# Kernel optimization log

Measured on AMD Instinct MI355X. Metric: run time of the kernel, lower is better.

## Reference

```python
import jax, jax.numpy as jnp
import numpy as np

N_HEADS = 16
EPS = 1e-5  # torch nn.LayerNorm default


def layernorm(x, g, b):
    mu = x.mean(-1, keepdims=True)
    var = ((x - mu) ** 2).mean(-1, keepdims=True)
    return (x - mu) * jax.lax.rsqrt(var + EPS) * g + b


def setup_inputs() -> dict:
    V, D, Dff, L, S, B = 32000, 1024, 4096, 6, 2048, 1
    key = jax.random.key(0)
    ks = jax.random.split(key, 12)
    std = 0.02  # GPT-2 init
    nrm = lambda k, shp: jax.random.normal(k, shp, jnp.float32) * std
    return {
        "tokens": jax.random.randint(ks[0], (B, S), 0, V),
        "tok_emb": nrm(ks[1], (V, D)),          # tied with lm head
        "pos_emb": nrm(ks[2], (S, D)),
        "Wq": nrm(ks[3], (L, D, D)), "bq": jnp.zeros((L, D)),
        "Wk": nrm(ks[4], (L, D, D)), "bk": jnp.zeros((L, D)),
        "Wv": nrm(ks[5], (L, D, D)), "bv": jnp.zeros((L, D)),
        "Wo": nrm(ks[6], (L, D, D)), "bo": jnp.zeros((L, D)),
        "ln1_g": jnp.ones((L, D)), "ln1_b": jnp.zeros((L, D)),
        "ln2_g": jnp.ones((L, D)), "ln2_b": jnp.zeros((L, D)),
        "W1": nrm(ks[7], (L, D, Dff)), "b1": jnp.zeros((L, Dff)),
        "W2": nrm(ks[8], (L, Dff, D)), "b2": jnp.zeros((L, D)),
        "lnf_g": jnp.ones((D,)), "lnf_b": jnp.zeros((D,)),
    }


def reference(tokens, tok_emb, pos_emb, Wq, bq, Wk, bk, Wv, bv, Wo, bo,
              ln1_g, ln1_b, ln2_g, ln2_b, W1, b1, W2, b2, lnf_g, lnf_b):
    B, S = tokens.shape
    D = tok_emb.shape[1]
    dk = D // N_HEADS
    scale = 1.0 / np.sqrt(dk)

    x = tok_emb[tokens] + pos_emb[:S][None]           # (B,S,D); dropout p=0 -> identity
    causal = jnp.tril(jnp.ones((S, S), bool))

    def block(x, p):
        wq, bq_, wk, bk_, wv, bv_, wo, bo_, g1, b1_, g2, b2_, w1, bf1, w2, bf2 = p
        # --- attention sublayer (pre-norm) ---
        h = layernorm(x, g1, b1_)
        q = (h @ wq + bq_).reshape(B, S, N_HEADS, dk)
        k = (h @ wk + bk_).reshape(B, S, N_HEADS, dk)
        v = (h @ wv + bv_).reshape(B, S, N_HEADS, dk)
        scores = jnp.einsum('bqhd,bkhd->bhqk', q, k) * scale
        scores = jnp.where(causal, scores, -jnp.inf)   # masked_fill(mask==0, -inf)
        attn = jax.nn.softmax(scores, axis=-1)
        ctx = jnp.einsum('bhqk,bkhd->bqhd', attn, v).reshape(B, S, D)
        x = x + ctx @ wo + bo_
        # --- FFN sublayer (pre-norm) ---
        h = layernorm(x, g2, b2_)
        x = x + jax.nn.gelu(h @ w1 + bf1, approximate=False) @ w2 + bf2
        return x, None

    x, _ = jax.lax.scan(
        block, x,
        (Wq, bq, Wk, bk, Wv, bv, Wo, bo, ln1_g, ln1_b, ln2_g, ln2_b, W1, b1, W2, b2))
    x = layernorm(x, lnf_g, lnf_b)
    logits = x @ tok_emb.T                             # tied lm head (no bias)
    return logits
```

## Files before the change

kernel.cpp:

```cpp
#include <hip/hip_runtime.h>
#include <hip/hip_bf16.h>
#include <cstdint>
#include <cstddef>


typedef __attribute__((ext_vector_type(4))) float  f32x4;
typedef __attribute__((ext_vector_type(8))) __bf16 bf16x8;
typedef __attribute__((ext_vector_type(4))) __bf16 bf16x4;

#define S_LEN 2048
#define DMODEL 1024
#define DFF 4096
#define NLAYER 6
#define NHEAD 16
#define DK 64
#define VOCAB 32000
#define MN (S_LEN * DMODEL)

__device__ __forceinline__ void gload_lds16(const void* g, void* l) {
    __builtin_amdgcn_global_load_lds(
        (__attribute__((address_space(1))) void*)(void*)(g),
        (__attribute__((address_space(3))) void*)(l), 16, 0, 0);
}

__device__ __forceinline__ void tr64_body(
    const float* __restrict__ inp, __bf16* __restrict__ outp,
    int K, int N, int n0, int k0, int t) {
    __shared__ float tile[64][65];
    const int lc = t & 15, rr = t >> 4;
#pragma unroll
    for (int i = 0; i < 4; ++i) {
        float4 v = *(const float4*)&inp[(size_t)(k0 + rr + i * 16) * N + n0 + lc * 4];
        tile[rr + i * 16][lc * 4 + 0] = v.x;
        tile[rr + i * 16][lc * 4 + 1] = v.y;
        tile[rr + i * 16][lc * 4 + 2] = v.z;
        tile[rr + i * 16][lc * 4 + 3] = v.w;
    }
    __syncthreads();
    const int a = t & 7, b = t >> 3;
#pragma unroll
    for (int j = 0; j < 2; ++j) {
        const int n = b + j * 32;
        bf16x8 o;
#pragma unroll
        for (int e = 0; e < 8; ++e) o[e] = (__bf16)tile[a * 8 + e][n];
        *(bf16x8*)&outp[(size_t)(n0 + n) * K + k0 + a * 8] = o;
    }
}

__global__ __launch_bounds__(256) void transpose_cvt64(
    const float* __restrict__ in, __bf16* __restrict__ out,
    int K, int N, size_t in_lstride, size_t out_lstride) {
    tr64_body(in + blockIdx.z * in_lstride, out + blockIdx.z * out_lstride,
              K, N, blockIdx.x * 64, blockIdx.y * 64, threadIdx.x);
}

__global__ __launch_bounds__(256) void transpose_qkvo(
    const float* __restrict__ Wq, const float* __restrict__ Wk,
    const float* __restrict__ Wv, const float* __restrict__ Wo,
    __bf16* __restrict__ wqkv_t, __bf16* __restrict__ wo_t) {
    const int z = blockIdx.z, mat = z & 3, l = z >> 2;
    const float* src =
        (mat == 0 ? Wq : mat == 1 ? Wk : mat == 2 ? Wv : Wo) +
        (size_t)l * 1024 * 1024;
    __bf16* dst = (mat < 3)
        ? wqkv_t + (size_t)l * 3072 * 1024 + (size_t)mat * 1024 * 1024
        : wo_t + (size_t)l * 1024 * 1024;
    tr64_body(src, dst, 1024, 1024, blockIdx.x * 64, blockIdx.y * 64, threadIdx.x);
}

__global__ __launch_bounds__(256) void cvt_bf16(
    const float* __restrict__ in, __bf16* __restrict__ out, long n4) {
    long i = (long)blockIdx.x * 256 + threadIdx.x;
    if (i >= n4) return;
    float4 v = ((const float4*)in)[i];
    bf16x4 o = {(__bf16)v.x, (__bf16)v.y, (__bf16)v.z, (__bf16)v.w};
    ((bf16x4*)out)[i] = o;
}

template <int NPART, int EMBED>
__global__ __launch_bounds__(256) void ln_kernel(
    float* __restrict__ x, const float* __restrict__ p,
    const float* __restrict__ g, const float* __restrict__ b,
    __bf16* __restrict__ out,
    const int* __restrict__ tokens, const float* __restrict__ te,
    const float* __restrict__ pe) {
    const int row = blockIdx.x, t = threadIdx.x;
    float4 v;
    if (EMBED) {
        const int tok = tokens[row];
        float4 a = ((const float4*)(te + (size_t)tok * DMODEL))[t];
        float4 q = ((const float4*)(pe + (size_t)row * DMODEL))[t];
        v = float4{a.x + q.x, a.y + q.y, a.z + q.z, a.w + q.w};
        ((float4*)(x + (size_t)row * DMODEL))[t] = v;
    } else {
        v = ((const float4*)(x + (size_t)row * DMODEL))[t];
    }
    if (NPART == 2) {
        float4 a0 = ((const float4*)(p + (size_t)row * DMODEL))[t];
        float4 a1 = ((const float4*)(p + MN + (size_t)row * DMODEL))[t];
        v.x += a0.x + a1.x;
        v.y += a0.y + a1.y;
        v.z += a0.z + a1.z;
        v.w += a0.w + a1.w;
        ((float4*)(x + (size_t)row * DMODEL))[t] = v;
    }
    float s  = v.x + v.y + v.z + v.w;
    float s2 = v.x * v.x + v.y * v.y + v.z * v.z + v.w * v.w;
#pragma unroll
    for (int off = 1; off < 64; off <<= 1) {
        s  += __shfl_xor(s, off);
        s2 += __shfl_xor(s2, off);
    }
    __shared__ float ss[4], ss2[4];
    const int wave = t >> 6;
    if ((t & 63) == 0) { ss[wave] = s; ss2[wave] = s2; }
    __syncthreads();
    s  = ss[0] + ss[1] + ss[2] + ss[3];
    s2 = ss2[0] + ss2[1] + ss2[2] + ss2[3];
    const float mu  = s * (1.0f / DMODEL);
    const float var = s2 * (1.0f / DMODEL) - mu * mu;
    const float rstd = rsqrtf(var + 1e-5f);
    float4 gg = ((const float4*)g)[t];
    float4 bb = ((const float4*)b)[t];
    __bf16* o = out + (size_t)row * DMODEL + t * 4;
    o[0] = (__bf16)((v.x - mu) * rstd * gg.x + bb.x);
    o[1] = (__bf16)((v.y - mu) * rstd * gg.y + bb.y);
    o[2] = (__bf16)((v.z - mu) * rstd * gg.z + bb.z);
    o[3] = (__bf16)((v.w - mu) * rstd * gg.w + bb.w);
}

template <int BM, int BN, int BK, int SPLITK, int MODE, int XCD>
__global__ __launch_bounds__(256) void gemm_tiled(
    const __bf16* __restrict__ A, const __bf16* __restrict__ BT,
    int M, int N, int K,
    const float* __restrict__ bias,
    float* __restrict__ fout,
    __bf16* __restrict__ bfout,
    __bf16* __restrict__ qb, __bf16* __restrict__ kb, __bf16* __restrict__ vb,
    const float* __restrict__ bq, const float* __restrict__ bk,
    const float* __restrict__ bv) {
    constexpr int SLOTS = BK / 8;
    constexpr int SH    = (BK == 64) ? 0 : 1;
    constexpr int RPC   = 2048 / BK;
    constexpr int ACH_A = BM / RPC;
    constexpr int ACH_B = BN / RPC;
    constexpr int LOADS = ACH_A + ACH_B;
    constexpr int MR = BM / 32;
    constexpr int NR = BN / 32;
    constexpr int KS = BK / 32;
    __shared__ alignas(16) __bf16 As[2][BM * BK];
    __shared__ alignas(16) __bf16 Bs[2][BN * BK];
    const int t = threadIdx.x;
    const int wave = t >> 6, lane = t & 63;
    const int wr = wave >> 1, wc = wave & 1;
    const int lg = lane >> 4, lr = lane & 15;

    int bx = blockIdx.x, by = blockIdx.y;
    if (XCD) {
        const int nwg = gridDim.x * gridDim.y;
        const int wgid = by * gridDim.x + bx;
        const int sw = (wgid & 7) * (nwg >> 3) + (wgid >> 3);
        bx = sw % gridDim.x;
        by = sw / gridDim.x;
    }
    const int row0 = bx * BM, col0 = by * BN;
    const int kz = (SPLITK > 1) ? blockIdx.z : 0;
    const int Ksl = K / SPLITK;

    f32x4 acc[MR][NR];
#pragma unroll
    for (int i = 0; i < MR; i++)
#pragma unroll
        for (int j = 0; j < NR; j++) acc[i][j] = f32x4{0.f, 0.f, 0.f, 0.f};

    const int srow = t / SLOTS;
    const int sks = ((t % SLOTS) ^ ((srow >> SH) & (SLOTS - 1))) * 8;
    const __bf16* Ab = A + (size_t)(row0 + srow) * K + kz * Ksl + sks;
    const __bf16* Bb = BT + (size_t)(col0 + srow) * K + kz * Ksl + sks;

    const int nt = Ksl / BK;
#pragma unroll
    for (int ch = 0; ch < ACH_A; ++ch)
        gload_lds16(Ab + (size_t)ch * RPC * K, &As[0][ch * 2048 + wave * 512]);
#pragma unroll
    for (int ch = 0; ch < ACH_B; ++ch)
        gload_lds16(Bb + (size_t)ch * RPC * K, &Bs[0][ch * 2048 + wave * 512]);

    int c = 0;
    for (int T = 0; T < nt; ++T) {
        if (T + 1 < nt) {
            const int k0 = (T + 1) * BK;
#pragma unroll
            for (int ch = 0; ch < ACH_A; ++ch)
                gload_lds16(Ab + (size_t)ch * RPC * K + k0,
                            &As[c ^ 1][ch * 2048 + wave * 512]);
#pragma unroll
            for (int ch = 0; ch < ACH_B; ++ch)
                gload_lds16(Bb + (size_t)ch * RPC * K + k0,
                            &Bs[c ^ 1][ch * 2048 + wave * 512]);
            if constexpr (LOADS == 3)
                asm volatile("s_waitcnt vmcnt(3)" ::: "memory");
            else if constexpr (LOADS == 4)
                asm volatile("s_waitcnt vmcnt(4)" ::: "memory");
            else if constexpr (LOADS == 6)
                asm volatile("s_waitcnt vmcnt(6)" ::: "memory");
            else
                asm volatile("s_waitcnt vmcnt(8)" ::: "memory");
        } else {
            asm volatile("s_waitcnt vmcnt(0)" ::: "memory");
        }
        __builtin_amdgcn_s_barrier();
        asm volatile("" ::: "memory");

        bf16x8 af[MR][KS], bfr[NR][KS];
#pragma unroll
        for (int i = 0; i < MR; i++)
#pragma unroll
            for (int ks = 0; ks < KS; ks++) {
                const int row = wr * (BM / 2) + i * 16 + lr;
                const int ph = ((ks * 4 + lg) ^ ((row >> SH) & (SLOTS - 1)));
                af[i][ks] = *(const bf16x8*)&As[c][row * BK + ph * 8];
            }
#pragma unroll
        for (int j = 0; j < NR; j++)
#pragma unroll
            for (int ks = 0; ks < KS; ks++) {
                const int n = wc * (BN / 2) + j * 16 + lr;
                const int ph = ((ks * 4 + lg) ^ ((n >> SH) & (SLOTS - 1)));
                bfr[j][ks] = *(const bf16x8*)&Bs[c][n * BK + ph * 8];
            }
        __builtin_amdgcn_s_setprio(1);
#pragma unroll
        for (int i = 0; i < MR; i++)
#pragma unroll
            for (int j = 0; j < NR; j++)
#pragma unroll
                for (int ks = 0; ks < KS; ks++)
                    acc[i][j] = __builtin_amdgcn_mfma_f32_16x16x32_bf16(
                        af[i][ks], bfr[j][ks], acc[i][j], 0, 0, 0);
        __builtin_amdgcn_s_setprio(0);
        asm volatile("" ::: "memory");
        __builtin_amdgcn_s_barrier();
        c ^= 1;
    }

#pragma unroll
    for (int i = 0; i < MR; i++) {
#pragma unroll
        for (int j = 0; j < NR; j++) {
#pragma unroll
            for (int r = 0; r < 4; r++) {
                const int row = row0 + wr * (BM / 2) + i * 16 + lg * 4 + r;
                const int col = col0 + wc * (BN / 2) + j * 16 + lr;
                float v = acc[i][j][r];
                if (MODE == 0) {
                    const int sec = col >> 10, cn = col & 1023;
                    const int head = cn >> 6, d = cn & 63;
                    if (sec == 0) {
                        v = (v + bq[cn]) * 0.18033688011112042f;
                        qb[((size_t)head * S_LEN + row) * DK + d] = (__bf16)v;
                    } else if (sec == 1) {
                        v = v + bk[cn];
                        kb[((size_t)head * S_LEN + row) * DK + d] = (__bf16)v;
                    } else {
                        v = v + bv[cn];
                        vb[((size_t)head * DK + d) * S_LEN + row] = (__bf16)v;
                    }
                } else if (MODE == 2) {
                    const float gg = v + bias[col];
                    const float cgl = 0.5f * gg * (1.0f + erff(gg * 0.70710678118654752f));
                    bfout[(size_t)row * N + col] = (__bf16)cgl;
                } else if (MODE == 6) {
                    const float vv = v + (kz == 0 ? bias[col] : 0.f);
                    __builtin_nontemporal_store(
                        vv, &fout[(size_t)kz * MN + (size_t)row * N + col]);
                } else {
                    __builtin_nontemporal_store(v, &fout[(size_t)row * N + col]);
                }
            }
        }
    }
}

__global__ __launch_bounds__(256) void attn_kernel(
    const __bf16* __restrict__ q, const __bf16* __restrict__ k,
    const __bf16* __restrict__ vt, __bf16* __restrict__ ctx) {
    const int xb = blockIdx.x, head = blockIdx.y;
    const int t = threadIdx.x;
    const int wave = t >> 6, lane = t & 63;
    const int lg = lane >> 4, lr = lane & 15;
    const int rg = (wave < 2) ? (2 * xb + wave) : (127 - 2 * xb - (3 - wave));
    const int rowbase = rg * 16;
    const int tend = rg >> 3;

    const __bf16* qh = q + (size_t)head * S_LEN * DK;
    const __bf16* kh = k + (size_t)head * S_LEN * DK;
    const __bf16* vh = vt + (size_t)head * DK * S_LEN;

    __shared__ alignas(16) __bf16 pls[4][16 * 136];
    __bf16* pw = pls[wave];

    bf16x8 qf0 = *(const bf16x8*)&qh[(size_t)(rowbase + lr) * DK + lg * 8];
    bf16x8 qf1 = *(const bf16x8*)&qh[(size_t)(rowbase + lr) * DK + 32 + lg * 8];

    f32x4 oacc[4];
#pragma unroll
    for (int j = 0; j < 4; j++) oacc[j] = f32x4{0.f, 0.f, 0.f, 0.f};
    float m[4], l[4];
#pragma unroll
    for (int r = 0; r < 4; r++) { m[r] = -__builtin_inff(); l[r] = 0.f; }

    for (int tt = 0; tt <= tend; ++tt) {
        const int kv0 = tt * 128;
        f32x4 sc[8];
        __builtin_amdgcn_s_setprio(1);
#pragma unroll
        for (int jn = 0; jn < 8; jn++) {
            bf16x8 kf0 = *(const bf16x8*)&kh[(size_t)(kv0 + jn * 16 + lr) * DK + lg * 8];
            bf16x8 kf1 = *(const bf16x8*)&kh[(size_t)(kv0 + jn * 16 + lr) * DK + 32 + lg * 8];
            sc[jn] = __builtin_amdgcn_mfma_f32_16x16x32_bf16(
                qf0, kf0, f32x4{0.f, 0.f, 0.f, 0.f}, 0, 0, 0);
            sc[jn] = __builtin_amdgcn_mfma_f32_16x16x32_bf16(qf1, kf1, sc[jn], 0, 0, 0);
        }
        __builtin_amdgcn_s_setprio(0);

        if (tt == tend) {
#pragma unroll
            for (int jn = 0; jn < 8; jn++)
#pragma unroll
                for (int r = 0; r < 4; r++) {
                    const int qrow = rowbase + lg * 4 + r;
                    if (kv0 + jn * 16 + lr > qrow) sc[jn][r] = -__builtin_inff();
                }
        }

        float mt[4];
#pragma unroll
        for (int r = 0; r < 4; r++) {
            float a0 = fmaxf(fmaxf(sc[0][r], sc[1][r]), fmaxf(sc[2][r], sc[3][r]));
            float a1 = fmaxf(fmaxf(sc[4][r], sc[5][r]), fmaxf(sc[6][r], sc[7][r]));
            mt[r] = fmaxf(a0, a1);
        }
#pragma unroll
        for (int off = 1; off < 16; off <<= 1)
#pragma unroll
            for (int r = 0; r < 4; r++) mt[r] = fmaxf(mt[r], __shfl_xor(mt[r], off));

        float alpha[4], psum[4];
#pragma unroll
        for (int r = 0; r < 4; r++) {
            const float mn = fmaxf(m[r], mt[r]);
            alpha[r] = exp2f(m[r] - mn);
            m[r] = mn;
#pragma unroll
            for (int jn = 0; jn < 8; jn++) sc[jn][r] = exp2f(sc[jn][r] - mn);
            psum[r] = ((sc[0][r] + sc[1][r]) + (sc[2][r] + sc[3][r])) +
                      ((sc[4][r] + sc[5][r]) + (sc[6][r] + sc[7][r]));
        }
#pragma unroll
        for (int off = 1; off < 16; off <<= 1)
#pragma unroll
            for (int r = 0; r < 4; r++) psum[r] += __shfl_xor(psum[r], off);
#pragma unroll
        for (int r = 0; r < 4; r++) l[r] = l[r] * alpha[r] + psum[r];
#pragma unroll
        for (int j = 0; j < 4; j++)
#pragma unroll
            for (int r = 0; r < 4; r++) oacc[j][r] *= alpha[r];

#pragma unroll
        for (int r = 0; r < 4; r++)
#pragma unroll
            for (int jn = 0; jn < 8; jn++)
                pw[(lg * 4 + r) * 136 + jn * 16 + lr] = (__bf16)sc[jn][r];

        bf16x8 pf[4];
#pragma unroll
        for (int h = 0; h < 4; h++)
            pf[h] = *(const bf16x8*)&pw[lr * 136 + h * 32 + lg * 8];
        __builtin_amdgcn_s_setprio(1);
#pragma unroll
        for (int j = 0; j < 4; j++) {
#pragma unroll
            for (int h = 0; h < 4; h++) {
                bf16x8 vf = *(const bf16x8*)
                    &vh[(size_t)(j * 16 + lr) * S_LEN + kv0 + h * 32 + lg * 8];
                oacc[j] = __builtin_amdgcn_mfma_f32_16x16x32_bf16(
                    pf[h], vf, oacc[j], 0, 0, 0);
            }
        }
        __builtin_amdgcn_s_setprio(0);
    }

#pragma unroll
    for (int j = 0; j < 4; j++)
#pragma unroll
        for (int r = 0; r < 4; r++) {
            const int row = rowbase + lg * 4 + r;
            ctx[(size_t)row * DMODEL + head * DK + j * 16 + lr] =
                (__bf16)(oacc[j][r] / l[r]);
        }
}

extern "C" void kernel_launch(void* const* d_in, const int* in_sizes, int n_in,
                              void* d_out, int out_size, void* d_ws, size_t ws_size,
                              hipStream_t stream) {
    const int*   tokens  = (const int*)d_in[0];
    const float* tok_emb = (const float*)d_in[1];
    const float* pos_emb = (const float*)d_in[2];
    const float* Wq = (const float*)d_in[3];
    const float* bq = (const float*)d_in[4];
    const float* Wk = (const float*)d_in[5];
    const float* bk = (const float*)d_in[6];
    const float* Wv = (const float*)d_in[7];
    const float* bv = (const float*)d_in[8];
    const float* Wo = (const float*)d_in[9];
    const float* bo = (const float*)d_in[10];
    const float* ln1_g = (const float*)d_in[11];
    const float* ln1_b = (const float*)d_in[12];
    const float* ln2_g = (const float*)d_in[13];
    const float* ln2_b = (const float*)d_in[14];
    const float* W1 = (const float*)d_in[15];
    const float* b1 = (const float*)d_in[16];
    const float* W2 = (const float*)d_in[17];
    const float* b2 = (const float*)d_in[18];
    const float* lnf_g = (const float*)d_in[19];
    const float* lnf_b = (const float*)d_in[20];

    char* ws = (char*)d_ws;
    size_t off = 0;
    auto alloc = [&](size_t bytes) {
        char* p = ws + off;
        off = (off + bytes + 255) & ~(size_t)255;
        return p;
    };
    __bf16* wqkv_t = (__bf16*)alloc((size_t)NLAYER * 3072 * 1024 * 2);
    __bf16* wo_t   = (__bf16*)alloc((size_t)NLAYER * 1024 * 1024 * 2);
    __bf16* w1_t   = (__bf16*)alloc((size_t)NLAYER * 4096 * 1024 * 2);
    __bf16* w2_t   = (__bf16*)alloc((size_t)NLAYER * 1024 * 4096 * 2);
    __bf16* temb   = (__bf16*)alloc((size_t)VOCAB * DMODEL * 2);
    float*  x      = (float*)alloc((size_t)MN * 4);
    __bf16* h      = (__bf16*)alloc((size_t)MN * 2);
    __bf16* qbuf   = (__bf16*)alloc((size_t)MN * 2);
    __bf16* kbuf   = (__bf16*)alloc((size_t)MN * 2);
    __bf16* vbuf   = (__bf16*)alloc((size_t)MN * 2);
    __bf16* ctx    = (__bf16*)alloc((size_t)MN * 2);
    __bf16* ffn    = (__bf16*)alloc((size_t)S_LEN * DFF * 2);
    if (off > ws_size) return;

    float* pproj  = (float*)ffn;
    float* pffn2  = (float*)qbuf;

    const dim3 blk256(256);

    transpose_qkvo<<<dim3(16, 16, 4 * NLAYER), blk256, 0, stream>>>(
        Wq, Wk, Wv, Wo, wqkv_t, wo_t);
    transpose_cvt64<<<dim3(64, 16, NLAYER), blk256, 0, stream>>>(
        W1, w1_t, 1024, 4096, (size_t)1024 * 4096, (size_t)4096 * 1024);
    transpose_cvt64<<<dim3(16, 64, NLAYER), blk256, 0, stream>>>(
        W2, w2_t, 4096, 1024, (size_t)4096 * 1024, (size_t)1024 * 4096);
    cvt_bf16<<<dim3((VOCAB * DMODEL / 4 + 255) / 256), blk256, 0, stream>>>(
        tok_emb, temb, (long)VOCAB * DMODEL / 4);

    ln_kernel<0, 1><<<dim3(S_LEN), blk256, 0, stream>>>(
        x, nullptr, ln1_g, ln1_b, h, tokens, tok_emb, pos_emb);

    for (int l = 0; l < NLAYER; ++l) {
        gemm_tiled<128, 128, 64, 1, 0, 0><<<dim3(16, 24), blk256, 0, stream>>>(
            h, wqkv_t + (size_t)l * 3072 * 1024, S_LEN, 3072, 1024,
            nullptr, nullptr, nullptr, qbuf, kbuf, vbuf,
            bq + l * 1024, bk + l * 1024, bv + l * 1024);
        attn_kernel<<<dim3(32, NHEAD), blk256, 0, stream>>>(
            qbuf, kbuf, vbuf, ctx);
        gemm_tiled<64, 128, 64, 2, 6, 0><<<dim3(32, 8, 2), blk256, 0, stream>>>(
            ctx, wo_t + (size_t)l * 1024 * 1024, S_LEN, 1024, 1024,
            bo + l * 1024, pproj, nullptr, nullptr, nullptr, nullptr,
            nullptr, nullptr, nullptr);
        ln_kernel<2, 0><<<dim3(S_LEN), blk256, 0, stream>>>(
            x, pproj, ln2_g + l * 1024, ln2_b + l * 1024, h,
            nullptr, nullptr, nullptr);
        gemm_tiled<128, 128, 64, 1, 2, 0><<<dim3(16, 32), blk256, 0, stream>>>(
            h, w1_t + (size_t)l * 4096 * 1024, S_LEN, 4096, 1024,
            b1 + l * 4096, nullptr, ffn, nullptr, nullptr, nullptr,
            nullptr, nullptr, nullptr);
        gemm_tiled<64, 128, 64, 2, 6, 0><<<dim3(32, 8, 2), blk256, 0, stream>>>(
            ffn, w2_t + (size_t)l * 1024 * 4096, S_LEN, 1024, 4096,
            b2 + l * 1024, pffn2, nullptr, nullptr, nullptr, nullptr,
            nullptr, nullptr, nullptr);
        if (l + 1 < NLAYER) {
            ln_kernel<2, 0><<<dim3(S_LEN), blk256, 0, stream>>>(
                x, pffn2, ln1_g + (l + 1) * 1024, ln1_b + (l + 1) * 1024, h,
                nullptr, nullptr, nullptr);
        }
    }

    ln_kernel<2, 0><<<dim3(S_LEN), blk256, 0, stream>>>(
        x, pffn2, lnf_g, lnf_b, h, nullptr, nullptr, nullptr);
    gemm_tiled<128, 256, 32, 1, 3, 1><<<dim3(16, 125), blk256, 0, stream>>>(
        h, temb, S_LEN, VOCAB, 1024,
        nullptr, (float*)d_out, nullptr, nullptr, nullptr, nullptr,
        nullptr, nullptr, nullptr);
}
```

Measured before the change: 1.598 ms.

## Use one barrier per K-step in GEMM and XCD-swizzle attention blocks

The GEMM main loop is restructured. It loads the first tile up front, issues the prefetch of the next tile before computing the current one, and waits for all loads plus a single barrier after the compute. This drops the second per-iteration barrier and the LOADS-dependent partial vmcnt waits. Separately, the attention kernel remaps its block index so consecutive blocks spread across XCDs, which should improve cache locality per head. The full vmcnt(0) wait at the end of each step may expose some memory latency if the compute is shorter than the loads.

```diff
diff --git a/kernel.cpp b/kernel.cpp
--- a/kernel.cpp
+++ b/kernel.cpp
@@ -145,7 +145,6 @@
     constexpr int RPC   = 2048 / BK;
     constexpr int ACH_A = BM / RPC;
     constexpr int ACH_B = BN / RPC;
-    constexpr int LOADS = ACH_A + ACH_B;
     constexpr int MR = BM / 32;
     constexpr int NR = BN / 32;
     constexpr int KS = BK / 32;
@@ -180,38 +179,29 @@
     const __bf16* Bb = BT + (size_t)(col0 + srow) * K + kz * Ksl + sks;
 
     const int nt = Ksl / BK;
-#pragma unroll
-    for (int ch = 0; ch < ACH_A; ++ch)
-        gload_lds16(Ab + (size_t)ch * RPC * K, &As[0][ch * 2048 + wave * 512]);
-#pragma unroll
-    for (int ch = 0; ch < ACH_B; ++ch)
-        gload_lds16(Bb + (size_t)ch * RPC * K, &Bs[0][ch * 2048 + wave * 512]);
+    auto stage = [&](int T, int buf) {
+        const int k0 = T * BK;
+#pragma unroll
+        for (int ch = 0; ch < ACH_A; ++ch)
+            gload_lds16(Ab + (size_t)ch * RPC * K + k0,
+                        &As[buf][ch * 2048 + wave * 512]);
+#pragma unroll
+        for (int ch = 0; ch < ACH_B; ++ch)
+            gload_lds16(Bb + (size_t)ch * RPC * K + k0,
+                        &Bs[buf][ch * 2048 + wave * 512]);
+    };
+
+    stage(0, 0);
+    asm volatile("s_waitcnt vmcnt(0)" ::: "memory");
+    __builtin_amdgcn_s_barrier();
+    asm volatile("" ::: "memory");
 
     int c = 0;
     for (int T = 0; T < nt; ++T) {
         if (T + 1 < nt) {
-            const int k0 = (T + 1) * BK;
-#pragma unroll
-            for (int ch = 0; ch < ACH_A; ++ch)
-                gload_lds16(Ab + (size_t)ch * RPC * K + k0,
-                            &As[c ^ 1][ch * 2048 + wave * 512]);
-#pragma unroll
-            for (int ch = 0; ch < ACH_B; ++ch)
-                gload_lds16(Bb + (size_t)ch * RPC * K + k0,
-                            &Bs[c ^ 1][ch * 2048 + wave * 512]);
-            if constexpr (LOADS == 3)
-                asm volatile("s_waitcnt vmcnt(3)" ::: "memory");
-            else if constexpr (LOADS == 4)
-                asm volatile("s_waitcnt vmcnt(4)" ::: "memory");
-            else if constexpr (LOADS == 6)
-                asm volatile("s_waitcnt vmcnt(6)" ::: "memory");
-            else
-                asm volatile("s_waitcnt vmcnt(8)" ::: "memory");
-        } else {
-            asm volatile("s_waitcnt vmcnt(0)" ::: "memory");
-        }
-        __builtin_amdgcn_s_barrier();
-        asm volatile("" ::: "memory");
+            stage(T + 1, c ^ 1);
+            asm volatile("" ::: "memory");
+        }
 
         bf16x8 af[MR][KS], bfr[NR][KS];
 #pragma unroll
@@ -240,8 +230,12 @@
                     acc[i][j] = __builtin_amdgcn_mfma_f32_16x16x32_bf16(
                         af[i][ks], bfr[j][ks], acc[i][j], 0, 0, 0);
         __builtin_amdgcn_s_setprio(0);
-        asm volatile("" ::: "memory");
-        __builtin_amdgcn_s_barrier();
+
+        if (T + 1 < nt) {
+            asm volatile("s_waitcnt vmcnt(0)" ::: "memory");
+            __builtin_amdgcn_s_barrier();
+            asm volatile("" ::: "memory");
+        }
         c ^= 1;
     }
 
@@ -286,7 +280,9 @@
 __global__ __launch_bounds__(256) void attn_kernel(
     const __bf16* __restrict__ q, const __bf16* __restrict__ k,
     const __bf16* __restrict__ vt, __bf16* __restrict__ ctx) {
-    const int xb = blockIdx.x, head = blockIdx.y;
+    const int lin = blockIdx.y * 32 + blockIdx.x;
+    const int u = (lin & 7) * 64 + (lin >> 3);
+    const int head = u >> 5, xb = u & 31;
     const int t = threadIdx.x;
     const int wave = t >> 6, lane = t & 63;
     const int lg = lane >> 4, lr = lane & 15;
```

New measurement: 1.615 ms. About the same (+1.1%).

## Add dedicated 256x256 triple-buffered logits GEMM and remap attention block order

Applied to the files above, without the earlier changes.

Replaces the generic tiled GEMM for the tied LM-head logits with a specialized 512-thread kernel. It uses 256x256 tiles, triple-buffered LDS filled by direct global-to-LDS loads, swizzled LDS layout, and block-ID remapping so that blocks sharing A/B tiles are grouped per XCD. Attention blocks are also remapped so heads are spread across XCDs for better L2 locality. The larger tile raises per-CU reuse but leaves 1000 blocks at one block per CU, which risks tail imbalance and register pressure.

```diff
diff --git a/kernel.cpp b/kernel.cpp
--- a/kernel.cpp
+++ b/kernel.cpp
@@ -283,10 +283,102 @@
     }
 }
 
+__global__ __launch_bounds__(512, 1) void gemm_logits_p3(
+    const __bf16* __restrict__ A, const __bf16* __restrict__ BT,
+    float* __restrict__ fout) {
+    constexpr int K = 1024, N = VOCAB, NT = 32;
+    __shared__ alignas(16) __bf16 As[3][256 * 32];
+    __shared__ alignas(16) __bf16 Bs[3][256 * 32];
+    const int t = threadIdx.x;
+    const int wv = t >> 6, lane = t & 63;
+    const int wm = wv >> 2, wn = wv & 3;
+    const int lg = lane >> 4, lr = lane & 15;
+
+    const int wgid = blockIdx.x;
+    const int sw = (wgid & 7) * 125 + (wgid >> 3);
+    const int row0 = (sw & 7) * 256;
+    const int col0 = (sw >> 3) * 256;
+
+    const int srl = wv * 32 + (lane >> 2);
+    const int sks = ((lane & 3) ^ ((srl >> 1) & 3)) * 8;
+    const __bf16* Asrc = A + (size_t)(row0 + srl) * K + sks;
+    const __bf16* Bsrc = BT + (size_t)(col0 + srl) * K + sks;
+
+    auto stage = [&](int T, int buf) {
+        const int k0 = T * 32;
+        gload_lds16(Asrc + k0,              &As[buf][(wv * 32) * 32]);
+        gload_lds16(Asrc + (size_t)16 * K + k0, &As[buf][(wv * 32 + 16) * 32]);
+        gload_lds16(Bsrc + k0,              &Bs[buf][(wv * 32) * 32]);
+        gload_lds16(Bsrc + (size_t)16 * K + k0, &Bs[buf][(wv * 32 + 16) * 32]);
+    };
+
+    f32x4 acc[8][4];
+#pragma unroll
+    for (int i = 0; i < 8; i++)
+#pragma unroll
+        for (int j = 0; j < 4; j++) acc[i][j] = f32x4{0.f, 0.f, 0.f, 0.f};
+
+    stage(0, 0);
+    stage(1, 1);
+    asm volatile("s_waitcnt vmcnt(4)" ::: "memory");
+    __builtin_amdgcn_s_barrier();
+    asm volatile("" ::: "memory");
+
+    int cb = 0, sb = 2;
+    for (int T = 0; T < NT; ++T) {
+        if (T + 2 < NT) stage(T + 2, sb);
+
+        const __bf16* Asl = As[cb];
+        const __bf16* Bsl = Bs[cb];
+        bf16x8 af[8], bfr[4];
+#pragma unroll
+        for (int i = 0; i < 8; i++) {
+            const int row = wm * 128 + i * 16 + lr;
+            af[i] = *(const bf16x8*)&Asl[row * 32 + ((lg ^ ((row >> 1) & 3)) * 8)];
+        }
+#pragma unroll
+        for (int j = 0; j < 4; j++) {
+            const int n = wn * 64 + j * 16 + lr;
+            bfr[j] = *(const bf16x8*)&Bsl[n * 32 + ((lg ^ ((n >> 1) & 3)) * 8)];
+        }
+        __builtin_amdgcn_s_setprio(1);
+#pragma unroll
+        for (int i = 0; i < 8; i++)
+#pragma unroll
+            for (int j = 0; j < 4; j++)
+                acc[i][j] = __builtin_amdgcn_mfma_f32_16x16x32_bf16(
+                    af[i], bfr[j], acc[i][j], 0, 0, 0);
+        __builtin_amdgcn_s_setprio(0);
+
+        if (T + 2 < NT)
+            asm volatile("s_waitcnt vmcnt(4)" ::: "memory");
+        else if (T + 1 < NT)
+            asm volatile("s_waitcnt vmcnt(0)" ::: "memory");
+        __builtin_amdgcn_s_barrier();
+        asm volatile("" ::: "memory");
+        cb = (cb == 2) ? 0 : cb + 1;
+        sb = (sb == 2) ? 0 : sb + 1;
+    }
+
+#pragma unroll
+    for (int i = 0; i < 8; i++)
+#pragma unroll
+        for (int j = 0; j < 4; j++)
+#pragma unroll
+            for (int r = 0; r < 4; r++) {
+                const int row = row0 + wm * 128 + i * 16 + lg * 4 + r;
+                const int col = col0 + wn * 64 + j * 16 + lr;
+                __builtin_nontemporal_store(acc[i][j][r],
+                                            &fout[(size_t)row * N + col]);
+            }
+}
+
 __global__ __launch_bounds__(256) void attn_kernel(
     const __bf16* __restrict__ q, const __bf16* __restrict__ k,
     const __bf16* __restrict__ vt, __bf16* __restrict__ ctx) {
-    const int xb = blockIdx.x, head = blockIdx.y;
+    const int lin = blockIdx.y * 32 + blockIdx.x;
+    const int u = (lin & 7) * 64 + (lin >> 3);
+    const int head = u >> 5, xb = u & 31;
     const int t = threadIdx.x;
     const int wave = t >> 6, lane = t & 63;
     const int lg = lane >> 4, lr = lane & 15;
@@ -497,8 +589,6 @@
 
     ln_kernel<2, 0><<<dim3(S_LEN), blk256, 0, stream>>>(
         x, pffn2, lnf_g, lnf_b, h, nullptr, nullptr, nullptr);
-    gemm_tiled<128, 256, 32, 1, 3, 1><<<dim3(16, 125), blk256, 0, stream>>>(
-        h, temb, S_LEN, VOCAB, 1024,
-        nullptr, (float*)d_out, nullptr, nullptr, nullptr, nullptr,
-        nullptr, nullptr, nullptr);
-}
+    gemm_logits_p3<<<dim3(1000), dim3(512), 0, stream>>>(
+        h, temb, (float*)d_out);
+}
```

Result: no change. 1.621 ms (median of 2 runs) (+1.4%).

## Add dedicated 256x256 eight-wave LM-head GEMM and remap attention block order

Applied to the files above, without the earlier changes.

Replaces the generic tiled GEMM for the tied LM head with a specialised 512-thread kernel. It uses 256x256 tiles, double-buffered direct global-to-LDS loads with XOR swizzle, and quarter-tile ping-pong scheduling that interleaves loads with MFMA bursts under setprio. Blocks are remapped so the 8 row tiles sharing a column tile run in adjacent groups, aiming for better L2 reuse of the embedding matrix. The attention kernel also gets a block-index swizzle spreading heads across XCDs. Large LDS use and launch_bounds(512,1) limit occupancy to one block per CU.

```diff
diff --git a/kernel.cpp b/kernel.cpp
--- a/kernel.cpp
+++ b/kernel.cpp
@@ -283,10 +283,167 @@
     }
 }
 
+__global__ __launch_bounds__(512, 1) void gemm_logits_8r(
+    const __bf16* __restrict__ A, const __bf16* __restrict__ BT,
+    float* __restrict__ fout) {
+    constexpr int K = 1024, N = VOCAB, NT = 16;
+    __shared__ alignas(16) __bf16 As[2][256 * 64];
+    __shared__ alignas(16) __bf16 Bs[2][256 * 64];
+    const int t = threadIdx.x;
+    const int wv = t >> 6, lane = t & 63;
+    const int pm = wv >> 2, pn = wv & 3;
+    const int lg = lane >> 4, lr = lane & 15;
+
+    const int wgid = blockIdx.x;
+    const int sw = (wgid & 7) * 125 + (wgid >> 3);
+    const int row0 = (sw & 7) * 256;
+    const int col0 = (sw >> 3) * 256;
+
+    const int srow = t >> 3;
+    const int sks = ((t & 7) ^ (srow & 7)) * 8;
+    const __bf16* Ab = A + (size_t)(row0 + srow) * K + sks;
+    const __bf16* Bb = BT + (size_t)(col0 + srow) * K + sks;
+
+    auto stA = [&](int T, int hf) {
+        const __bf16* g = Ab + (size_t)(hf * 128) * K + T * 64;
+        gload_lds16(g, &As[T & 1][(hf * 128 + wv * 8) * 64]);
+        gload_lds16(g + (size_t)64 * K, &As[T & 1][(hf * 128 + 64 + wv * 8) * 64]);
+    };
+    auto stB = [&](int T, int hf) {
+        const __bf16* g = Bb + (size_t)(hf * 128) * K + T * 64;
+        gload_lds16(g, &Bs[T & 1][(hf * 128 + wv * 8) * 64]);
+        gload_lds16(g + (size_t)64 * K, &Bs[T & 1][(hf * 128 + 64 + wv * 8) * 64]);
+    };
+
+    f32x4 acc[4][4][2];
+#pragma unroll
+    for (int p = 0; p < 4; p++)
+#pragma unroll
+        for (int i = 0; i < 4; i++)
+#pragma unroll
+            for (int j = 0; j < 2; j++) acc[p][i][j] = f32x4{0.f, 0.f, 0.f, 0.f};
+
+    bf16x8 af[4][2], bfr[2][2];
+    auto loadA = [&](int b, int ah) {
+#pragma unroll
+        for (int il = 0; il < 4; il++)
+#pragma unroll
+            for (int ks = 0; ks < 2; ks++) {
+                const int row = ah * 128 + pm * 64 + il * 16 + lr;
+                af[il][ks] = *(const bf16x8*)
+                    &As[b][row * 64 + (((ks * 4 + lg) ^ (row & 7)) * 8)];
+            }
+    };
+    auto loadB = [&](int b, int bh) {
+#pragma unroll
+        for (int jl = 0; jl < 2; jl++)
+#pragma unroll
+            for (int ks = 0; ks < 2; ks++) {
+                const int n = bh * 128 + pn * 32 + jl * 16 + lr;
+                bfr[jl][ks] = *(const bf16x8*)
+                    &Bs[b][n * 64 + (((ks * 4 + lg) ^ (n & 7)) * 8)];
+            }
+    };
+
+    stA(0, 0); stB(0, 0); stA(0, 1); stB(0, 1);
+    asm volatile("s_waitcnt vmcnt(4)" ::: "memory");
+    __builtin_amdgcn_s_barrier();
+    asm volatile("" ::: "memory");
+
+    for (int T = 0; T < NT; ++T) {
+        const int b = T & 1;
+        const bool pf = (T + 1 < NT);
+
+        loadA(b, 0); loadB(b, 0);
+        if (pf) stA(T + 1, 0);
+        __builtin_amdgcn_s_setprio(1);
+#pragma unroll
+        for (int il = 0; il < 4; il++)
+#pragma unroll
+            for (int jl = 0; jl < 2; jl++)
+#pragma unroll
+                for (int ks = 0; ks < 2; ks++)
+                    acc[0][il][jl] = __builtin_amdgcn_mfma_f32_16x16x32_bf16(
+                        af[il][ks], bfr[jl][ks], acc[0][il][jl], 0, 0, 0);
+        __builtin_amdgcn_s_setprio(0);
+        if (pf) asm volatile("s_waitcnt vmcnt(4)" ::: "memory");
+        else    asm volatile("s_waitcnt vmcnt(2)" ::: "memory");
+        __builtin_amdgcn_s_barrier();
+        asm volatile("" ::: "memory");
+
+        loadA(b, 1);
+        if (pf) stB(T + 1, 0);
+        __builtin_amdgcn_s_setprio(1);
+#pragma unroll
+        for (int il = 0; il < 4; il++)
+#pragma unroll
+            for (int jl = 0; jl < 2; jl++)
+#pragma unroll
+                for (int ks = 0; ks < 2; ks++)
+                    acc[1][il][jl] = __builtin_amdgcn_mfma_f32_16x16x32_bf16(
+                        af[il][ks], bfr[jl][ks], acc[1][il][jl], 0, 0, 0);
+        __builtin_amdgcn_s_setprio(0);
+        if (pf) asm volatile("s_waitcnt vmcnt(4)" ::: "memory");
+        else    asm volatile("s_waitcnt vmcnt(0)" ::: "memory");
+        __builtin_amdgcn_s_barrier();
+        asm volatile("" ::: "memory");
+
+        loadB(b, 1);
+        if (pf) stA(T + 1, 1);
+        __builtin_amdgcn_s_setprio(1);
+#pragma unroll
+        for (int il = 0; il < 4; il++)
+#pragma unroll
+            for (int jl = 0; jl < 2; jl++)
+#pragma unroll
+                for (int ks = 0; ks < 2; ks++)
+                    acc[2][il][jl] = __builtin_amdgcn_mfma_f32_16x16x32_bf16(
+                        af[il][ks], bfr[jl][ks], acc[2][il][jl], 0, 0, 0);
+        __builtin_amdgcn_s_setprio(0);
+
+        loadA(b, 0);
+        if (pf) stB(T + 1, 1);
+        __builtin_amdgcn_s_setprio(1);
+#pragma unroll
+        for (int il = 0; il < 4; il++)
+#pragma unroll
+            for (int jl = 0; jl < 2; jl++)
+#pragma unroll
+                for (int ks = 0; ks < 2; ks++)
+                    acc[3][il][jl] = __builtin_amdgcn_mfma_f32_16x16x32_bf16(
+                        af[il][ks], bfr[jl][ks], acc[3][il][jl], 0, 0, 0);
+        __builtin_amdgcn_s_setprio(0);
+        if (pf) {
+            asm volatile("s_waitcnt vmcnt(4)" ::: "memory");
+            __builtin_amdgcn_s_barrier();
+            asm volatile("" ::: "memory");
+        }
+    }
+
+#pragma unroll
+    for (int p = 0; p < 4; p++) {
+        const int ah = (p == 1 || p == 2) ? 1 : 0;
+        const int bh = (p >= 2) ? 1 : 0;
+#pragma unroll
+        for (int il = 0; il < 4; il++)
+#pragma unroll
+            for (int jl = 0; jl < 2; jl++)
+#pragma unroll
+                for (int r = 0; r < 4; r++) {
+                    const int row = row0 + ah * 128 + pm * 64 + il * 16 + lg * 4 + r;
+                    const int col = col0 + bh * 128 + pn * 32 + jl * 16 + lr;
+                    __builtin_nontemporal_store(acc[p][il][jl][r],
+                                                &fout[(size_t)row * N + col]);
+                }
+    }
+}
+
 __global__ __launch_bounds__(256) void attn_kernel(
     const __bf16* __restrict__ q, const __bf16* __restrict__ k,
     const __bf16* __restrict__ vt, __bf16* __restrict__ ctx) {
-    const int xb = blockIdx.x, head = blockIdx.y;
+    const int lin = blockIdx.y * 32 + blockIdx.x;
+    const int u = (lin & 7) * 64 + (lin >> 3);
+    const int head = u >> 5, xb = u & 31;
     const int t = threadIdx.x;
     const int wave = t >> 6, lane = t & 63;
     const int lg = lane >> 4, lr = lane & 15;
@@ -497,8 +654,6 @@
 
     ln_kernel<2, 0><<<dim3(S_LEN), blk256, 0, stream>>>(
         x, pffn2, lnf_g, lnf_b, h, nullptr, nullptr, nullptr);
-    gemm_tiled<128, 256, 32, 1, 3, 1><<<dim3(16, 125), blk256, 0, stream>>>(
-        h, temb, S_LEN, VOCAB, 1024,
-        nullptr, (float*)d_out, nullptr, nullptr, nullptr, nullptr,
-        nullptr, nullptr, nullptr);
-}
+    gemm_logits_8r<<<dim3(1000), dim3(512), 0, stream>>>(
+        h, temb, (float*)d_out);
+}
```

After: 1.633 ms, median of 2. 1.02x slower.
